# Kernel optimization log

Measured on AMD Instinct MI355X. Metric: run time of the kernel, lower is better.

## Reference

```python
import jax, jax.numpy as jnp
import numpy as np

B, T, N = 512, 1024, 64


def setup_inputs() -> dict:
    key = jax.random.key(0)
    k1, k2, k3, k4 = jax.random.split(key, 4)
    inputs = jax.random.normal(k1, (B, T, N), dtype=jnp.float32)
    trans = jax.random.normal(k2, (N, N), dtype=jnp.float32) * 0.1
    tag_indices = jax.random.randint(k3, (B, T), 0, N)
    sequence_lengths = jax.random.randint(k4, (B,), 1, T + 1)  # at least 1
    return {
        "inputs": inputs,
        "trans": trans,
        "tag_indices": tag_indices,
        "sequence_lengths": sequence_lengths,
    }


def _crf_log_likelihood(inputs, trans, tag_indices, sequence_lengths):
    Bn, Tn, Nn = inputs.shape
    # mask[b, t] = 1 if t < length[b]
    mask = (jnp.arange(Tn)[None, :] < sequence_lengths[:, None]).astype(inputs.dtype)

    # unary score: sum_t inputs[b, t, tag[b, t]] * mask
    unary = jnp.take_along_axis(inputs, tag_indices[..., None], axis=2)[..., 0]  # [B, T]
    unary_score = jnp.sum(unary * mask, axis=1)

    # binary score: sum_t trans[tag[t], tag[t+1]] masked by mask[:, 1:]
    binary = trans[tag_indices[:, :-1], tag_indices[:, 1:]]  # [B, T-1]
    binary_score = jnp.sum(binary * mask[:, 1:], axis=1)

    sequence_scores = unary_score + binary_score

    # log normalizer via forward algorithm (logsumexp recurrence)
    first = inputs[:, 0]                       # [B, N] initial alphas
    rest = jnp.swapaxes(inputs[:, 1:], 0, 1)   # [T-1, B, N] time-major
    steps = jnp.arange(Tn - 1)

    def step(alpha, xt):
        x, t = xt  # x: [B, N]
        # alpha[b, i] + trans[i, j], logsumexp over i
        new = x + jax.nn.logsumexp(alpha[:, :, None] + trans[None, :, :], axis=1)
        # dynamic_rnn with sequence_length = len - 1: stop updating past the end
        upd = (t < sequence_lengths - 1)[:, None]
        return jnp.where(upd, new, alpha), None

    alpha, _ = jax.lax.scan(step, first, (rest, steps))
    log_norm = jax.nn.logsumexp(alpha, axis=1)  # [B]

    return sequence_scores - log_norm


def reference(inputs, trans, tag_indices, sequence_lengths):
    return _crf_log_likelihood(inputs, trans, tag_indices, sequence_lengths)
```

## Files before the change

### kernel.cpp

```cpp
#include <hip/hip_runtime.h>
#include <math.h>

#define Bn 512
#define Tn 1024
#define Nn 64
#define LOG2E_F 1.44269504088896340736f
#define LN2_F   0.69314718055994530942f

typedef __attribute__((ext_vector_type(2))) float f32x2;

__device__ __forceinline__ float wave_max(float v) {
    #pragma unroll
    for (int o = 32; o > 0; o >>= 1) v = fmaxf(v, __shfl_xor(v, o));
    return v;
}
__device__ __forceinline__ float wave_sum(float v) {
    #pragma unroll
    for (int o = 32; o > 0; o >>= 1) v += __shfl_xor(v, o);
    return v;
}


#define STEP2(BWDV, EXV) do {                                      \
    shq[j] = (BWDV) ? ((EXV) * q) : q;                             \
    f32x2 _a0 = {0.f, 0.f}, _a1 = {0.f, 0.f};                      \
    f32x2 _a2 = {0.f, 0.f}, _a3 = {0.f, 0.f};                      \
    _Pragma("unroll")                                              \
    for (int _cb = 0; _cb < 8; ++_cb) {                            \
        float4 _qv = *(const float4*)&shq[(g << 5) + (_cb << 2)];  \
        _a0 = __builtin_elementwise_fma((f32x2){_qv.x, _qv.x}, EfPQ[4*_cb + 0], _a0); \
        _a1 = __builtin_elementwise_fma((f32x2){_qv.y, _qv.y}, EfPQ[4*_cb + 1], _a1); \
        _a2 = __builtin_elementwise_fma((f32x2){_qv.z, _qv.z}, EfPQ[4*_cb + 2], _a2); \
        _a3 = __builtin_elementwise_fma((f32x2){_qv.w, _qv.w}, EfPQ[4*_cb + 3], _a3); \
    }                                                              \
    f32x2 _s2 = (_a0 + _a1) + (_a2 + _a3);                         \
    float _u = lo32 ? _s2[0] : _s2[1];                             \
    float _w = lo32 ? _s2[1] : _s2[0];                             \
    float _s = _u + __shfl_xor(_w, 32);                            \
    q = (BWDV) ? _s : ((EXV) * _s);                                \
} while (0)

__device__ __forceinline__ int clamp_row(int tt, int Lm1) {
    return tt < 0 ? 0 : (tt > Lm1 ? Lm1 : tt);
}

template <bool FULL>
__global__ __launch_bounds__(64, 1) void crf_main(
    const float* __restrict__ inputs, const float* __restrict__ trans,
    const int* __restrict__ tags, const int* __restrict__ lens,
    float* __restrict__ ws, float* __restrict__ out)
{
    const int j = threadIdx.x;

    if (!FULL && blockIdx.x >= 2 * Bn) {
        const int b = blockIdx.x - 2 * Bn;
        const int L = lens[b];
        const int* tagb = tags + b * Tn;
        const float* inb = inputs + (size_t)b * Tn * Nn;
        float sacc = 0.f;
        #pragma unroll
        for (int i = 0; i < Tn / 64; ++i) {
            int t  = j + 64 * i;
            int tm = t > 0 ? t - 1 : 0;
            int tg = tagb[t];
            int tp = tagb[tm];
            float un = inb[t * Nn + tg];
            float bi = trans[tp * Nn + tg];
            float c  = un + ((t >= 1) ? bi : 0.f);
            sacc += (t < L) ? c : 0.f;
        }
        float sc = wave_sum(sacc);
        if (j == 0) out[b] = sc;
        return;
    }

    const int g = j >> 5;
    const int p = j & 31;
    const bool lo32 = (j < 32);
    const bool bwd = (!FULL) && (blockIdx.x >= Bn);
    const int b = bwd ? (blockIdx.x - Bn) : blockIdx.x;
    const int L = lens[b];
    const int Lm1 = L - 1;
    const float* inb = inputs + (size_t)b * Tn * Nn;

    f32x2 EfPQ[32];
    __shared__ float trsh[64 * 65];
    __shared__ __align__(16) float shq[64];
    if (!bwd) {
        #pragma unroll
        for (int c = 0; c < 32; ++c) {
            EfPQ[c][0] = exp2f(trans[(g * 32 + c) * 64 + p     ] * LOG2E_F);
            EfPQ[c][1] = exp2f(trans[(g * 32 + c) * 64 + p + 32] * LOG2E_F);
        }
    } else {
        #pragma unroll
        for (int i = 0; i < 64; ++i) trsh[i * 65 + j] = trans[i * 64 + j];
        __syncthreads();
        #pragma unroll
        for (int c = 0; c < 32; ++c) {
            EfPQ[c][0] = exp2f(trsh[p        * 65 + g * 32 + c] * LOG2E_F);
            EfPQ[c][1] = exp2f(trsh[(p + 32) * 65 + g * 32 + c] * LOG2E_F);
        }
    }

    float q, base;
    int t0, dir, n;
    const int tf = L >> 1;
    if (!bwd) {
        float x0 = inb[j];
        float m = wave_max(x0);
        q = exp2f((x0 - m) * LOG2E_F);
        base = m;
        t0 = 1; dir = 1;
        n = FULL ? (L - 1) : tf;
    } else {
        q = 1.f; base = 0.f;
        t0 = L - 1; dir = -1;
        n = (L - 1) - tf;
    }

    float xc[8];
    #pragma unroll
    for (int d = 0; d < 8; ++d)
        xc[d] = inb[clamp_row(t0 + d * dir, Lm1) * Nn + j];

    int t = t0;
    int k = 0;
    float pend = 1.0f;

    if (!bwd) {
        while (k + 8 <= n) {
            float xn[8];
            #pragma unroll
            for (int d = 0; d < 8; ++d)
                xn[d] = inb[clamp_row(t + (8 + d) * dir, Lm1) * Nn + j];
            float exc[8];
            #pragma unroll
            for (int u = 0; u < 8; ++u)
                exc[u] = exp2f(fmaf(xc[u], LOG2E_F, -6.0f));
            exc[2] *= pend;
            #pragma unroll
            for (int u = 0; u < 8; ++u) STEP2(false, exc[u]);
            float m = wave_max(q);
            base += __logf(m);
            pend = 1.0f / m;
            #pragma unroll
            for (int d = 0; d < 8; ++d) xc[d] = xn[d];
            k += 8; t += 8;
        }
        q *= pend; pend = 1.0f;
        #pragma unroll
        for (int u = 0; u < 8; ++u) {
            if (k + u < n) {
                float exu = exp2f(fmaf(xc[u], LOG2E_F, -6.0f));
                STEP2(false, exu);
            }
        }
    } else {
        while (k + 8 <= n) {
            float xn[8];
            #pragma unroll
            for (int d = 0; d < 8; ++d)
                xn[d] = inb[clamp_row(t - (8 + d), Lm1) * Nn + j];
            float exc[8];
            #pragma unroll
            for (int u = 0; u < 8; ++u)
                exc[u] = exp2f(fmaf(xc[u], LOG2E_F, -6.0f));
            exc[2] *= pend;
            #pragma unroll
            for (int u = 0; u < 8; ++u) STEP2(true, exc[u]);
            float m = wave_max(q);
            base += __logf(m);
            pend = 1.0f / m;
            #pragma unroll
            for (int d = 0; d < 8; ++d) xc[d] = xn[d];
            k += 8; t -= 8;
        }
        q *= pend; pend = 1.0f;
        #pragma unroll
        for (int u = 0; u < 8; ++u) {
            if (k + u < n) {
                float exu = exp2f(fmaf(xc[u], LOG2E_F, -6.0f));
                STEP2(true, exu);
            }
        }
    }

    {
        float m = wave_max(q);
        q *= (1.0f / m);
        base += __logf(m) + LN2_F * 6.0f * (float)n;
    }

    if (FULL) {
        float ssum = wave_sum(q);
        if (j == 0) out[b] -= (base + __logf(ssum));
    } else {
        float* fvec = ws;
        float* gvec = ws + Bn * 64;
        float* fb   = ws + 2 * Bn * 64;
        float* gb   = fb + Bn;
        if (!bwd) { fvec[b * 64 + j] = q; if (j == 0) fb[b] = base; }
        else      { gvec[b * 64 + j] = q; if (j == 0) gb[b] = base; }
    }
}

__global__ __launch_bounds__(256) void crf_scores(
    const float* __restrict__ inputs, const float* __restrict__ trans,
    const int* __restrict__ tags, const int* __restrict__ lens,
    float* __restrict__ out)
{
    const int b = blockIdx.x;
    const int L = lens[b];
    const int* tagb = tags + b * Tn;
    const float* inb = inputs + (size_t)b * Tn * Nn;

    float acc = 0.f;
    for (int t = threadIdx.x; t < L; t += 256) {
        int tg = tagb[t];
        acc += inb[t * Nn + tg];
        if (t >= 1) acc += trans[tagb[t - 1] * Nn + tg];
    }
    acc = wave_sum(acc);
    __shared__ float red[4];
    if ((threadIdx.x & 63) == 0) red[threadIdx.x >> 6] = acc;
    __syncthreads();
    if (threadIdx.x == 0) out[b] = (red[0] + red[1]) + (red[2] + red[3]);
}

__global__ __launch_bounds__(64, 1) void crf_combine(
    const float* __restrict__ ws, float* __restrict__ out)
{
    const int b = blockIdx.x;
    const int j = threadIdx.x;
    const float* fvec = ws;
    const float* gvec = ws + Bn * 64;
    const float* fb   = ws + 2 * Bn * 64;
    const float* gb   = fb + Bn;

    float p = wave_sum(fvec[b * 64 + j] * gvec[b * 64 + j]);
    if (j == 0) out[b] -= (__logf(p) + fb[b] + gb[b]);
}

extern "C" void kernel_launch(void* const* d_in, const int* in_sizes, int n_in,
                              void* d_out, int out_size, void* d_ws, size_t ws_size,
                              hipStream_t stream) {
    const float* inputs = (const float*)d_in[0];
    const float* trans  = (const float*)d_in[1];
    const int*   tags   = (const int*)d_in[2];
    const int*   lens   = (const int*)d_in[3];
    float* out = (float*)d_out;
    float* ws  = (float*)d_ws;

    const size_t need = (size_t)(2 * Bn * 64 + 2 * Bn) * sizeof(float);
    if (ws_size >= need) {
        crf_main<false><<<3 * Bn, 64, 0, stream>>>(inputs, trans, tags, lens, ws, out);
        crf_combine<<<Bn, 64, 0, stream>>>(ws, out);
    } else {
        crf_scores<<<Bn, 256, 0, stream>>>(inputs, trans, tags, lens, out);
        crf_main<true><<<Bn, 64, 0, stream>>>(inputs, trans, tags, lens, ws, out);
    }
}
```

Baseline: 323.8 us.

## Run forward and backward CRF recurrences interleaved in one wavefront per sequence

Instead of separate blocks for the forward and backward halves of the alpha recurrence, each block now runs both chains, interleaving their steps so two independent dependency chains hide each other's LDS/shuffle latency. The dot-product combine happens in-kernel, shrinking workspace and replacing the combine kernel with a tiny subtraction kernel. This halves the number of recurrence waves and doubles per-wave register use (two 64-entry transition arrays), which may cause spills and lowers available parallelism across CUs.

```diff
diff --git a/kernel.cpp b/kernel.cpp
--- a/kernel.cpp
+++ b/kernel.cpp
@@ -7,8 +7,6 @@
 #define LOG2E_F 1.44269504088896340736f
 #define LN2_F   0.69314718055994530942f
 
-typedef __attribute__((ext_vector_type(2))) float f32x2;
-
 __device__ __forceinline__ float wave_max(float v) {
     #pragma unroll
     for (int o = 32; o > 0; o >>= 1) v = fmaxf(v, __shfl_xor(v, o));
@@ -21,23 +19,35 @@
 }
 
 
-#define STEP2(BWDV, EXV) do {                                      \
-    shq[j] = (BWDV) ? ((EXV) * q) : q;                             \
-    f32x2 _a0 = {0.f, 0.f}, _a1 = {0.f, 0.f};                      \
-    f32x2 _a2 = {0.f, 0.f}, _a3 = {0.f, 0.f};                      \
+#define STEPD(QV, SH, EF, BWDV, EXV) do {                          \
+    SH[j] = (BWDV) ? ((EXV) * QV) : QV;                            \
+    float _aP0 = 0.f, _aP1 = 0.f, _aQ0 = 0.f, _aQ1 = 0.f;         \
     _Pragma("unroll")                                              \
-    for (int _cb = 0; _cb < 8; ++_cb) {                            \
-        float4 _qv = *(const float4*)&shq[(g << 5) + (_cb << 2)];  \
-        _a0 = __builtin_elementwise_fma((f32x2){_qv.x, _qv.x}, EfPQ[4*_cb + 0], _a0); \
-        _a1 = __builtin_elementwise_fma((f32x2){_qv.y, _qv.y}, EfPQ[4*_cb + 1], _a1); \
-        _a2 = __builtin_elementwise_fma((f32x2){_qv.z, _qv.z}, EfPQ[4*_cb + 2], _a2); \
-        _a3 = __builtin_elementwise_fma((f32x2){_qv.w, _qv.w}, EfPQ[4*_cb + 3], _a3); \
+    for (int _cb = 0; _cb < 8; _cb += 2) {                         \
+        const float4 _u0 = *(const float4*)&SH[(g << 5) + (_cb << 2)];      \
+        const float4 _u1 = *(const float4*)&SH[(g << 5) + ((_cb + 1) << 2)];\
+        _aP0 = fmaf(_u0.x, EF[4*_cb + 0], _aP0);                   \
+        _aQ0 = fmaf(_u0.x, EF[32 + 4*_cb + 0], _aQ0);              \
+        _aP0 = fmaf(_u0.y, EF[4*_cb + 1], _aP0);                   \
+        _aQ0 = fmaf(_u0.y, EF[32 + 4*_cb + 1], _aQ0);              \
+        _aP0 = fmaf(_u0.z, EF[4*_cb + 2], _aP0);                   \
+        _aQ0 = fmaf(_u0.z, EF[32 + 4*_cb + 2], _aQ0);              \
+        _aP0 = fmaf(_u0.w, EF[4*_cb + 3], _aP0);                   \
+        _aQ0 = fmaf(_u0.w, EF[32 + 4*_cb + 3], _aQ0);              \
+        _aP1 = fmaf(_u1.x, EF[4*_cb + 4], _aP1);                   \
+        _aQ1 = fmaf(_u1.x, EF[32 + 4*_cb + 4], _aQ1);              \
+        _aP1 = fmaf(_u1.y, EF[4*_cb + 5], _aP1);                   \
+        _aQ1 = fmaf(_u1.y, EF[32 + 4*_cb + 5], _aQ1);              \
+        _aP1 = fmaf(_u1.z, EF[4*_cb + 6], _aP1);                   \
+        _aQ1 = fmaf(_u1.z, EF[32 + 4*_cb + 6], _aQ1);              \
+        _aP1 = fmaf(_u1.w, EF[4*_cb + 7], _aP1);                   \
+        _aQ1 = fmaf(_u1.w, EF[32 + 4*_cb + 7], _aQ1);              \
     }                                                              \
-    f32x2 _s2 = (_a0 + _a1) + (_a2 + _a3);                         \
-    float _u = lo32 ? _s2[0] : _s2[1];                             \
-    float _w = lo32 ? _s2[1] : _s2[0];                             \
+    float _aP = _aP0 + _aP1, _aQ = _aQ0 + _aQ1;                    \
+    float _u = lo32 ? _aP : _aQ;                                   \
+    float _w = lo32 ? _aQ : _aP;                                   \
     float _s = _u + __shfl_xor(_w, 32);                            \
-    q = (BWDV) ? _s : ((EXV) * _s);                                \
+    QV = (BWDV) ? _s : ((EXV) * _s);                               \
 } while (0)
 
 __device__ __forceinline__ int clamp_row(int tt, int Lm1) {
@@ -52,8 +62,8 @@
 {
     const int j = threadIdx.x;
 
-    if (!FULL && blockIdx.x >= 2 * Bn) {
-        const int b = blockIdx.x - 2 * Bn;
+    if (!FULL && blockIdx.x >= Bn) {
+        const int b = blockIdx.x - Bn;
         const int L = lens[b];
         const int* tagb = tags + b * Tn;
         const float* inb = inputs + (size_t)b * Tn * Nn;
@@ -70,139 +80,160 @@
             sacc += (t < L) ? c : 0.f;
         }
         float sc = wave_sum(sacc);
-        if (j == 0) out[b] = sc;
+        if (j == 0) ws[Bn + b] = sc;
         return;
     }
 
     const int g = j >> 5;
     const int p = j & 31;
     const bool lo32 = (j < 32);
-    const bool bwd = (!FULL) && (blockIdx.x >= Bn);
-    const int b = bwd ? (blockIdx.x - Bn) : blockIdx.x;
+    const int b = blockIdx.x;
     const int L = lens[b];
     const int Lm1 = L - 1;
     const float* inb = inputs + (size_t)b * Tn * Nn;
 
-    f32x2 EfPQ[32];
     __shared__ float trsh[64 * 65];
-    __shared__ __align__(16) float shq[64];
-    if (!bwd) {
-        #pragma unroll
-        for (int c = 0; c < 32; ++c) {
-            EfPQ[c][0] = exp2f(trans[(g * 32 + c) * 64 + p     ] * LOG2E_F);
-            EfPQ[c][1] = exp2f(trans[(g * 32 + c) * 64 + p + 32] * LOG2E_F);
-        }
-    } else {
+    __shared__ __align__(16) float shqF[64];
+    __shared__ __align__(16) float shqB[64];
+
+    float EfF[64];
+    #pragma unroll
+    for (int c = 0; c < 32; ++c) {
+        EfF[c]      = exp2f(trans[(g * 32 + c) * 64 + p     ] * LOG2E_F);
+        EfF[32 + c] = exp2f(trans[(g * 32 + c) * 64 + p + 32] * LOG2E_F);
+    }
+    float EfB[64];
+    if (!FULL) {
         #pragma unroll
         for (int i = 0; i < 64; ++i) trsh[i * 65 + j] = trans[i * 64 + j];
         __syncthreads();
         #pragma unroll
         for (int c = 0; c < 32; ++c) {
-            EfPQ[c][0] = exp2f(trsh[p        * 65 + g * 32 + c] * LOG2E_F);
-            EfPQ[c][1] = exp2f(trsh[(p + 32) * 65 + g * 32 + c] * LOG2E_F);
-        }
-    }
-
-    float q, base;
-    int t0, dir, n;
-    const int tf = L >> 1;
-    if (!bwd) {
+            EfB[c]      = exp2f(trsh[p        * 65 + g * 32 + c] * LOG2E_F);
+            EfB[32 + c] = exp2f(trsh[(p + 32) * 65 + g * 32 + c] * LOG2E_F);
+        }
+    }
+
+    float qf, basef;
+    {
         float x0 = inb[j];
         float m = wave_max(x0);
-        q = exp2f((x0 - m) * LOG2E_F);
-        base = m;
-        t0 = 1; dir = 1;
-        n = FULL ? (L - 1) : tf;
-    } else {
-        q = 1.f; base = 0.f;
-        t0 = L - 1; dir = -1;
-        n = (L - 1) - tf;
-    }
-
-    float xc[8];
-    #pragma unroll
-    for (int d = 0; d < 8; ++d)
-        xc[d] = inb[clamp_row(t0 + d * dir, Lm1) * Nn + j];
-
-    int t = t0;
-    int k = 0;
-    float pend = 1.0f;
-
-    if (!bwd) {
-        while (k + 8 <= n) {
+        qf = exp2f((x0 - m) * LOG2E_F);
+        basef = m;
+    }
+    const int tf = L >> 1;
+    const int nf = FULL ? Lm1 : tf;
+    const int nb = FULL ? 0 : (Lm1 - tf);
+
+    float qb = 1.f, baseb = 0.f;
+
+    float xcf[8], xcb[8];
+    #pragma unroll
+    for (int d = 0; d < 8; ++d) {
+        xcf[d] = inb[clamp_row(1 + d, Lm1) * Nn + j];
+        xcb[d] = inb[clamp_row(Lm1 - d, Lm1) * Nn + j];
+    }
+
+    int k = 0, tA = 1, tB = Lm1;
+    float pendf = 1.0f, pendb = 1.0f;
+
+    if (FULL) {
+        while (k + 8 <= nf) {
             float xn[8];
             #pragma unroll
             for (int d = 0; d < 8; ++d)
-                xn[d] = inb[clamp_row(t + (8 + d) * dir, Lm1) * Nn + j];
+                xn[d] = inb[clamp_row(tA + 8 + d, Lm1) * Nn + j];
             float exc[8];
             #pragma unroll
             for (int u = 0; u < 8; ++u)
-                exc[u] = exp2f(fmaf(xc[u], LOG2E_F, -6.0f));
-            exc[2] *= pend;
-            #pragma unroll
-            for (int u = 0; u < 8; ++u) STEP2(false, exc[u]);
-            float m = wave_max(q);
-            base += __logf(m);
-            pend = 1.0f / m;
-            #pragma unroll
-            for (int d = 0; d < 8; ++d) xc[d] = xn[d];
-            k += 8; t += 8;
-        }
-        q *= pend; pend = 1.0f;
+                exc[u] = exp2f(fmaf(xcf[u], LOG2E_F, -6.0f));
+            exc[2] *= pendf;
+            #pragma unroll
+            for (int u = 0; u < 8; ++u) STEPD(qf, shqF, EfF, false, exc[u]);
+            float m = wave_max(qf);
+            basef += __logf(m);
+            pendf = 1.0f / m;
+            #pragma unroll
+            for (int d = 0; d < 8; ++d) xcf[d] = xn[d];
+            k += 8; tA += 8;
+        }
+        qf *= pendf;
         #pragma unroll
         for (int u = 0; u < 8; ++u) {
-            if (k + u < n) {
-                float exu = exp2f(fmaf(xc[u], LOG2E_F, -6.0f));
-                STEP2(false, exu);
+            if (k + u < nf) {
+                float exu = exp2f(fmaf(xcf[u], LOG2E_F, -6.0f));
+                STEPD(qf, shqF, EfF, false, exu);
             }
         }
-    } else {
-        while (k + 8 <= n) {
-            float xn[8];
-            #pragma unroll
-            for (int d = 0; d < 8; ++d)
-                xn[d] = inb[clamp_row(t - (8 + d), Lm1) * Nn + j];
-            float exc[8];
-            #pragma unroll
-            for (int u = 0; u < 8; ++u)
-                exc[u] = exp2f(fmaf(xc[u], LOG2E_F, -6.0f));
-            exc[2] *= pend;
-            #pragma unroll
-            for (int u = 0; u < 8; ++u) STEP2(true, exc[u]);
-            float m = wave_max(q);
-            base += __logf(m);
-            pend = 1.0f / m;
-            #pragma unroll
-            for (int d = 0; d < 8; ++d) xc[d] = xn[d];
-            k += 8; t -= 8;
-        }
-        q *= pend; pend = 1.0f;
+        float m = wave_max(qf);
+        qf *= (1.0f / m);
+        basef += __logf(m) + LN2_F * 6.0f * (float)nf;
+        float ssum = wave_sum(qf);
+        if (j == 0) out[b] -= (basef + __logf(ssum));
+        return;
+    }
+
+    while (k + 8 <= nb) {
+        float xnf[8], xnb[8];
+        #pragma unroll
+        for (int d = 0; d < 8; ++d) {
+            xnf[d] = inb[clamp_row(tA + 8 + d, Lm1) * Nn + j];
+            xnb[d] = inb[clamp_row(tB - (8 + d), Lm1) * Nn + j];
+        }
+        float excf[8], excb[8];
         #pragma unroll
         for (int u = 0; u < 8; ++u) {
-            if (k + u < n) {
-                float exu = exp2f(fmaf(xc[u], LOG2E_F, -6.0f));
-                STEP2(true, exu);
-            }
+            excf[u] = exp2f(fmaf(xcf[u], LOG2E_F, -6.0f));
+            excb[u] = exp2f(fmaf(xcb[u], LOG2E_F, -6.0f));
+        }
+        excf[2] *= pendf;
+        excb[2] *= pendb;
+        #pragma unroll
+        for (int u = 0; u < 8; ++u) {
+            STEPD(qf, shqF, EfF, false, excf[u]);
+            STEPD(qb, shqB, EfB, true,  excb[u]);
+        }
+        float mf = wave_max(qf);
+        basef += __logf(mf); pendf = 1.0f / mf;
+        float mb = wave_max(qb);
+        baseb += __logf(mb); pendb = 1.0f / mb;
+        #pragma unroll
+        for (int d = 0; d < 8; ++d) { xcf[d] = xnf[d]; xcb[d] = xnb[d]; }
+        k += 8; tA += 8; tB -= 8;
+    }
+    qf *= pendf; qb *= pendb;
+    #pragma unroll
+    for (int u = 0; u < 8; ++u) {
+        if (k + u < nf) {
+            float exu = exp2f(fmaf(xcf[u], LOG2E_F, -6.0f));
+            STEPD(qf, shqF, EfF, false, exu);
+        }
+    }
+    #pragma unroll
+    for (int u = 0; u < 8; ++u) {
+        if (k + u < nb) {
+            float exu = exp2f(fmaf(xcb[u], LOG2E_F, -6.0f));
+            STEPD(qb, shqB, EfB, true, exu);
         }
     }
 
     {
-        float m = wave_max(q);
-        q *= (1.0f / m);
-        base += __logf(m) + LN2_F * 6.0f * (float)n;
-    }
-
-    if (FULL) {
-        float ssum = wave_sum(q);
-        if (j == 0) out[b] -= (base + __logf(ssum));
-    } else {
-        float* fvec = ws;
-        float* gvec = ws + Bn * 64;
-        float* fb   = ws + 2 * Bn * 64;
-        float* gb   = fb + Bn;
-        if (!bwd) { fvec[b * 64 + j] = q; if (j == 0) fb[b] = base; }
-        else      { gvec[b * 64 + j] = q; if (j == 0) gb[b] = base; }
-    }
+        float mf = wave_max(qf);
+        qf *= (1.0f / mf);
+        basef += __logf(mf) + LN2_F * 6.0f * (float)nf;
+        float mb = wave_max(qb);
+        qb *= (1.0f / mb);
+        baseb += __logf(mb) + LN2_F * 6.0f * (float)nb;
+        float dot = wave_sum(qf * qb);
+        if (j == 0) ws[b] = basef + baseb + __logf(dot);
+    }
+}
+
+__global__ __launch_bounds__(64) void crf_comb2(
+    const float* __restrict__ ws, float* __restrict__ out)
+{
+    const int idx = blockIdx.x * 64 + threadIdx.x;
+    if (idx < Bn) out[idx] = ws[Bn + idx] - ws[idx];
 }
 
 __global__ __launch_bounds__(256) void crf_scores(
@@ -228,20 +259,6 @@
     if (threadIdx.x == 0) out[b] = (red[0] + red[1]) + (red[2] + red[3]);
 }
 
-__global__ __launch_bounds__(64, 1) void crf_combine(
-    const float* __restrict__ ws, float* __restrict__ out)
-{
-    const int b = blockIdx.x;
-    const int j = threadIdx.x;
-    const float* fvec = ws;
-    const float* gvec = ws + Bn * 64;
-    const float* fb   = ws + 2 * Bn * 64;
-    const float* gb   = fb + Bn;
-
-    float p = wave_sum(fvec[b * 64 + j] * gvec[b * 64 + j]);
-    if (j == 0) out[b] -= (__logf(p) + fb[b] + gb[b]);
-}
-
 extern "C" void kernel_launch(void* const* d_in, const int* in_sizes, int n_in,
                               void* d_out, int out_size, void* d_ws, size_t ws_size,
                               hipStream_t stream) {
@@ -252,10 +269,10 @@
     float* out = (float*)d_out;
     float* ws  = (float*)d_ws;
 
-    const size_t need = (size_t)(2 * Bn * 64 + 2 * Bn) * sizeof(float);
+    const size_t need = (size_t)(2 * Bn) * sizeof(float);
     if (ws_size >= need) {
-        crf_main<false><<<3 * Bn, 64, 0, stream>>>(inputs, trans, tags, lens, ws, out);
-        crf_combine<<<Bn, 64, 0, stream>>>(ws, out);
+        crf_main<false><<<2 * Bn, 64, 0, stream>>>(inputs, trans, tags, lens, ws, out);
+        crf_comb2<<<(Bn + 63) / 64, 64, 0, stream>>>(ws, out);
     } else {
         crf_scores<<<Bn, 256, 0, stream>>>(inputs, trans, tags, lens, out);
         crf_main<true><<<Bn, 64, 0, stream>>>(inputs, trans, tags, lens, ws, out);
```

After: 402.2 us. 24.2% more time.
